# Kernel optimization log

Measured on AMD Instinct MI355X. Metric: run time of the kernel, lower is better.

Reference implementation:

```python
import jax, jax.numpy as jnp
import numpy as np

DX = 8e-6      # pixel pitch (m)
Z = 0.05       # propagation distance (m)
B, C, H, W = 8, 3, 1024, 1024


def setup_inputs() -> dict:
    key = jax.random.key(0)
    k1, k2 = jax.random.split(key)
    x_real = jax.random.normal(k1, (B, C, H, W), dtype=jnp.float32)
    x_imag = jax.random.normal(k2, (B, C, H, W), dtype=jnp.float32)
    wavelengths = jnp.asarray([450e-9, 532e-9, 632.8e-9], dtype=jnp.float32)
    return {"x_real": x_real, "x_imag": x_imag, "wavelengths": wavelengths}


def _transfer_function(wavelengths, h, w, dx, z):
    # Angular-spectrum transfer function per wavelength: [C, H, W] complex64
    fx = jnp.fft.fftfreq(w, d=dx).astype(jnp.float32)  # [W]
    fy = jnp.fft.fftfreq(h, d=dx).astype(jnp.float32)  # [H]
    f2 = fy[:, None] ** 2 + fx[None, :] ** 2           # [H, W]
    lam = wavelengths[:, None, None]                   # [C, 1, 1]
    arg = 1.0 - (lam ** 2) * f2[None]                  # [C, H, W]
    kz = (2.0 * jnp.pi / lam) * z * jnp.sqrt(jnp.maximum(arg, 0.0))
    Hc = jnp.exp(1j * kz.astype(jnp.complex64))
    # zero out evanescent components
    return jnp.where(arg > 0.0, Hc, jnp.zeros((), dtype=jnp.complex64))


def reference(x_real, x_imag, wavelengths):
    # Batched angular-spectrum propagation, one wavelength per channel.
    x = (x_real + 1j * x_imag).astype(jnp.complex64)   # [B, C, H, W]
    Hc = _transfer_function(wavelengths, H, W, DX, Z)  # [C, H, W]
    Xf = jnp.fft.fft2(x, axes=(-2, -1))
    out = jnp.fft.ifft2(Xf * Hc[None], axes=(-2, -1))  # [B, C, H, W] complex
    # return real/imag stacked so output is a float tensor: [2, B, C, H, W]
    return jnp.stack([out.real.astype(jnp.float32), out.imag.astype(jnp.float32)], axis=0)
```

## Files before the change

### kernel.cpp

```cpp
#include <hip/hip_runtime.h>
#include <math.h>


#define NIMG 24

__device__ __forceinline__ float2 cadd(float2 a, float2 b){ return make_float2(a.x+b.x, a.y+b.y); }
__device__ __forceinline__ float2 csub(float2 a, float2 b){ return make_float2(a.x-b.x, a.y-b.y); }
__device__ __forceinline__ float2 cmul(float2 a, float c, float s){ return make_float2(a.x*c - a.y*s, a.x*s + a.y*c); }

__device__ __forceinline__ int SW(int j) {
    int b = j << 3;
    return b ^ (((b >> 7) & 7) << 4);
}

__device__ __forceinline__ float2 computeH(float lam, int ky, int kx) {
    int iy = (ky < 512) ? ky : ky - 1024;
    int ix = (kx < 512) ? kx : kx - 1024;
    const double recip = 1.0 / (1024.0 * 8e-06);
    float fy = (float)((double)iy * recip);
    float fx = (float)((double)ix * recip);
    float f2  = __fadd_rn(__fmul_rn(fy, fy), __fmul_rn(fx, fx));
    float l2  = __fmul_rn(lam, lam);
    float arg = __fsub_rn(1.0f, __fmul_rn(l2, f2));
    float2 h = make_float2(0.0f, 0.0f);
    if (arg > 0.0f) {
        float t  = __fdiv_rn(6.28318530717958647692f, lam);
        t        = __fmul_rn(t, 0.05f);
        float kz = __fmul_rn(t, __fsqrt_rn(arg));
        double s, c;
        sincos((double)kz, &s, &c);
        const float sc = 9.5367431640625e-07f;
        h = make_float2((float)c * sc, (float)s * sc);
    }
    return h;
}

__global__ __launch_bounds__(256) void build_H_T(float2* __restrict__ Htab,
                                                 const float* __restrict__ wl) {
    int idx = blockIdx.x * 256 + threadIdx.x;
    int c   = idx >> 20;
    int rem = idx & 1048575;
    Htab[idx] = computeH(wl[c], rem & 1023, rem >> 10);
}

template<int SIGN>
__device__ __forceinline__ void dft4nt(float2& a0, float2& a1, float2& a2, float2& a3) {
    float2 t0 = cadd(a0, a2), t1 = csub(a0, a2);
    float2 t2 = cadd(a1, a3), t3 = csub(a1, a3);
    a0 = cadd(t0, t2);
    a2 = csub(t0, t2);
    a1 = make_float2(t1.x - SIGN * t3.y, t1.y + SIGN * t3.x);
    a3 = make_float2(t1.x + SIGN * t3.y, t1.y - SIGN * t3.x);
}
template<int SIGN>
__device__ __forceinline__ void dft4(float2& a0, float2& a1, float2& a2, float2& a3,
                                     float c1, float s1) {
    float c2 = c1*c1 - s1*s1, s2 = 2.f*c1*s1;
    float c3 = c2*c1 - s2*s1, s3 = s2*c1 + c2*s1;
    a1 = cmul(a1, c1, s1);
    a2 = cmul(a2, c2, s2);
    a3 = cmul(a3, c3, s3);
    dft4nt<SIGN>(a0, a1, a2, a3);
}

#define WSYNC() do { asm volatile("s_waitcnt lgkmcnt(0)" ::: "memory"); \
                     __builtin_amdgcn_wave_barrier(); } while (0)


__device__ __forceinline__ void ldsToRegs(char* cb, int l, float2 (&v)[4][4]) {
    const int swzE = (((l >> 4)    ) & 7) << 4;
    const int swzO = (((l >> 4) + 4) & 7) << 4;
    char* rbE = cb + ((8 * l) ^ swzE);
    char* rbO = cb + ((8 * l) ^ swzO);
    #pragma unroll
    for (int k = 0; k < 4; ++k) {
        #pragma unroll
        for (int r = 0; r < 4; ++r) {
            const int tt = k + 4 * r;
            v[k][r] = *(const float2*)(((tt & 1) ? rbO : rbE) + 512 * tt);
        }
    }
}
__device__ __forceinline__ void regsToLds(char* cb, int l, const float2 (&v)[4][4]) {
    const int swzE = (((l >> 4)    ) & 7) << 4;
    const int swzO = (((l >> 4) + 4) & 7) << 4;
    char* rbE = cb + ((8 * l) ^ swzE);
    char* rbO = cb + ((8 * l) ^ swzO);
    #pragma unroll
    for (int m = 0; m < 4; ++m) {
        #pragma unroll
        for (int q = 0; q < 4; ++q) {
            const int tt = m + 4 * q;
            *(float2*)(((tt & 1) ? rbO : rbE) + 512 * tt) = v[m][q];
        }
    }
}

template<int SIGN>
__device__ __forceinline__ void fftA(char* cb, int l, float2 (&v)[4][4]) {
    const float SPI8 = SIGN * 0.39269908169872415481f;
    #pragma unroll
    for (int k = 0; k < 4; ++k) dft4nt<SIGN>(v[k][0], v[k][1], v[k][2], v[k][3]);
    dft4nt<SIGN>(v[0][0], v[1][0], v[2][0], v[3][0]);
    #pragma unroll
    for (int q = 1; q < 4; ++q) {
        float s1, c1; __sincosf((float)q * SPI8, &s1, &c1);
        dft4<SIGN>(v[0][q], v[1][q], v[2][q], v[3][q], c1, s1);
    }
    char* wb = cb + 128 * l;
    const int L7 = l & 7;
    #pragma unroll
    for (int p = 0; p < 4; ++p) {
        *(float4*)(wb + 16 * ((2*p+0) ^ L7)) =
            make_float4(v[p][0].x, v[p][0].y, v[p][1].x, v[p][1].y);
        *(float4*)(wb + 16 * ((2*p+1) ^ L7)) =
            make_float4(v[p][2].x, v[p][2].y, v[p][3].x, v[p][3].y);
    }
}

template<int SIGN>
__device__ __forceinline__ void fftB(char* cb, int l) {
    const float SPI32  = SIGN * 0.09817477042468103870f;
    const float SPI128 = SIGN * 0.02454369260617025967f;
    const int swzE = (((l >> 4)    ) & 7) << 4;
    const int swzO = (((l >> 4) + 4) & 7) << 4;
    char* rbE = cb + ((8 * l) ^ swzE);
    char* rbO = cb + ((8 * l) ^ swzO);
    float2 v[4][4];
    #pragma unroll
    for (int k = 0; k < 4; ++k) {
        #pragma unroll
        for (int r = 0; r < 4; ++r) {
            const int tt = k + 4 * r;
            v[k][r] = *(const float2*)(((tt & 1) ? rbO : rbE) + 512 * tt);
        }
    }
    const int jm2 = l & 15;
    float s1, c1; __sincosf((float)jm2 * SPI32, &s1, &c1);
    #pragma unroll
    for (int k = 0; k < 4; ++k) dft4<SIGN>(v[k][0], v[k][1], v[k][2], v[k][3], c1, s1);
    const int lo8 = 8 * (l & 15);
    const int hi  = 2048 * (l >> 4);
    #pragma unroll
    for (int q = 0; q < 4; ++q) {
        float s1b, c1b; __sincosf((float)(jm2 + 16 * q) * SPI128, &s1b, &c1b);
        dft4<SIGN>(v[0][q], v[1][q], v[2][q], v[3][q], c1b, s1b);
        #pragma unroll
        for (int p = 0; p < 4; ++p) {
            const int K = ((q + 4 * p) & 7) << 4;
            *(float2*)(cb + (lo8 ^ K) + hi + 128 * q + 512 * p) = v[p][q];
        }
    }
}

template<int SIGN>
__device__ __forceinline__ void fftC(int l, float2 (&v)[4][4]) {
    const float SPI512 = SIGN * 0.00613592315154256492f;
    #pragma unroll
    for (int m = 0; m < 4; ++m) {
        float s1, c1; __sincosf((float)(l + 64 * m) * SPI512, &s1, &c1);
        dft4<SIGN>(v[m][0], v[m][1], v[m][2], v[m][3], c1, s1);
    }
}

__global__ __launch_bounds__(1024) void k1_rows_T16(const float* __restrict__ xr,
                                                    const float* __restrict__ xi,
                                                    float2* __restrict__ T) {
    extern __shared__ char lds[];
    const int t = threadIdx.x, w = t >> 6, l = t & 63;
    const int img = blockIdx.x >> 6;
    const int y0  = (blockIdx.x & 63) << 4;
    const long long ib = (long long)img << 20;
    char* cb = lds + 8192 * w;

    const float* rr = xr + ib + (long long)(y0 + w) * 1024;
    const float* ri = xi + ib + (long long)(y0 + w) * 1024;
    float2 v[4][4];
    #pragma unroll
    for (int k = 0; k < 4; ++k) {
        #pragma unroll
        for (int r = 0; r < 4; ++r) {
            const int p = l + 64 * (k + 4 * r);
            v[k][r] = make_float2(rr[p], ri[p]);
        }
    }
    fftA<-1>(cb, l, v); WSYNC();
    fftB<-1>(cb, l);    WSYNC();
    ldsToRegs(cb, l, v);
    fftC<-1>(l, v);
    __syncthreads();

    {
        const int w8 = w << 3;
        #pragma unroll
        for (int m = 0; m < 4; ++m) {
            #pragma unroll
            for (int q = 0; q < 4; ++q) {
                const int p  = l + 64 * (m + 4 * q);
                const int sx = (((p >> 1) & 7) << 4) | (((p >> 4) & 1) << 3);
                *(float2*)(lds + p * 128 + (w8 ^ sx)) = v[m][q];
            }
        }
    }
    __syncthreads();

    {
        const int j = l >> 3;
        const int xbase = (w << 3) + (l & 7);
        const bool sw = (w >> 1) & 1;
        #pragma unroll
        for (int i = 0; i < 8; ++i) {
            const int x   = xbase + (i << 7);
            const int s70 = ((x >> 1) & 7) << 4;
            float4 g = *(const float4*)(lds + x * 128 + ((16 * j) ^ s70));
            if (sw) g = make_float4(g.z, g.w, g.x, g.y);
            *(float4*)(T + ib + (long long)x * 1024 + y0 + 2 * j) = g;
        }
    }
}

__global__ __launch_bounds__(256, 4) void k2_cols_H(float2* __restrict__ T,
                                                    const float2* __restrict__ Htab,
                                                    const float* __restrict__ wl) {
    __shared__ float4 ldsb[2048];
    char* lds = (char*)ldsb;
    const int t = threadIdx.x, w = t >> 6, l = t & 63;
    const int img = blockIdx.x >> 8;
    const int x   = ((blockIdx.x & 255) << 2) + w;
    const int lamIdx = img % 3;
    char* cb = lds + 8192 * w;
    float2* col = T + ((long long)img << 20) + (long long)x * 1024;

    float2 v[4][4];
    #pragma unroll
    for (int k = 0; k < 4; ++k) {
        #pragma unroll
        for (int r = 0; r < 4; ++r)
            v[k][r] = col[l + 64 * (k + 4 * r)];
    }
    fftA<-1>(cb, l, v); WSYNC();
    fftB<-1>(cb, l);    WSYNC();

    float2 h[4][4];
    if (Htab) {
        const float2* hrow = Htab + ((long long)lamIdx << 20) + (long long)x * 1024;
        #pragma unroll
        for (int m = 0; m < 4; ++m) {
            #pragma unroll
            for (int q = 0; q < 4; ++q)
                h[m][q] = hrow[l + 64 * (m + 4 * q)];
        }
    } else {
        const float lam = wl[lamIdx];
        #pragma unroll
        for (int m = 0; m < 4; ++m) {
            #pragma unroll
            for (int q = 0; q < 4; ++q)
                h[m][q] = computeH(lam, l + 64 * (m + 4 * q), x);
        }
    }

    ldsToRegs(cb, l, v);
    fftC<-1>(l, v);

    #pragma unroll
    for (int m = 0; m < 4; ++m) {
        #pragma unroll
        for (int q = 0; q < 4; ++q) {
            float2 a = v[m][q], hh = h[m][q];
            v[m][q] = make_float2(a.x * hh.x - a.y * hh.y, a.x * hh.y + a.y * hh.x);
        }
    }
    WSYNC();

    fftA<1>(cb, l, v); WSYNC();
    fftB<1>(cb, l);    WSYNC();
    ldsToRegs(cb, l, v);
    fftC<1>(l, v);

    #pragma unroll
    for (int m = 0; m < 4; ++m) {
        #pragma unroll
        for (int q = 0; q < 4; ++q)
            col[l + 64 * (m + 4 * q)] = v[m][q];
    }
}

__global__ __launch_bounds__(1024) void k3_irows_T16(const float2* __restrict__ T,
                                                     float* __restrict__ outr,
                                                     float* __restrict__ outi) {
    extern __shared__ char lds[];
    const int t = threadIdx.x, w = t >> 6, l = t & 63;
    const int img = blockIdx.x >> 6;
    const int y0  = (blockIdx.x & 63) << 4;
    const long long ib = (long long)img << 20;

    {
        const float4* src = (const float4*)(T + ib + (long long)t * 1024 + y0);
        const int sx = SW(t);
        #pragma unroll
        for (int p = 0; p < 8; ++p) {
            float4 g = src[p];
            *(float2*)(lds + 8192 * (2 * p)     + sx) = make_float2(g.x, g.y);
            *(float2*)(lds + 8192 * (2 * p + 1) + sx) = make_float2(g.z, g.w);
        }
    }
    __syncthreads();

    char* cb = lds + 8192 * w;
    float2 v[4][4];
    ldsToRegs(cb, l, v);
    fftA<1>(cb, l, v); WSYNC();
    fftB<1>(cb, l);    WSYNC();
    ldsToRegs(cb, l, v);
    fftC<1>(l, v);

    float* pr = outr + ib + (long long)(y0 + w) * 1024;
    float* pi = outi + ib + (long long)(y0 + w) * 1024;
    #pragma unroll
    for (int m = 0; m < 4; ++m) {
        #pragma unroll
        for (int q = 0; q < 4; ++q) {
            const int p = l + 64 * (m + 4 * q);
            pr[p] = v[m][q].x;
            pi[p] = v[m][q].y;
        }
    }
}

extern "C" void kernel_launch(void* const* d_in, const int* in_sizes, int n_in,
                              void* d_out, int out_size, void* d_ws, size_t ws_size,
                              hipStream_t stream) {
    const float* xr = (const float*)d_in[0];
    const float* xi = (const float*)d_in[1];
    const float* wl = (const float*)d_in[2];
    float* out = (float*)d_out;

    const size_t planeElems = (size_t)NIMG * 1024 * 1024;
    float2* wsC = (float2*)d_ws;
    const size_t needC = planeElems * sizeof(float2);
    const size_t needH = (size_t)3 * 1024 * 1024 * sizeof(float2);
    float2* Htab = nullptr;
    if (ws_size >= needC + needH) {
        Htab = (float2*)((char*)d_ws + needC);
        build_H_T<<<12288, 256, 0, stream>>>(Htab, wl);
    }
    k1_rows_T16<<<NIMG * 64, 1024, 131072, stream>>>(xr, xi, wsC);
    k2_cols_H<<<NIMG * 256, 256, 0, stream>>>(wsC, Htab, wl);
    k3_irows_T16<<<NIMG * 64, 1024, 131072, stream>>>(wsC, out, out + planeElems);
}
```

Measured before the change: 304.2 us.

## Rotate 16-element row blocks in intermediate buffer to spread memory channels

The intermediate transposed buffer T now stores each 16-element block of a column at a position rotated by the column index, (b0 + x) & 63, instead of at y0. All three kernels are updated to match: the row-FFT writer, the column-FFT reader/writer via a CIDX mapping, and the inverse-row reader. The aim is to stop the strided transposed writes and reads from hitting the same memory channels or banks at the same time (partition camping). In exchange it adds index arithmetic, and the column kernel's loads become less regular, which could hurt coalescing within a wave.

Measured after the change: 350.2 us. 1.15x slower.

```diff
diff --git a/kernel.cpp b/kernel.cpp
--- a/kernel.cpp
+++ b/kernel.cpp
@@ -81,20 +81,6 @@
         }
     }
 }
-__device__ __forceinline__ void regsToLds(char* cb, int l, const float2 (&v)[4][4]) {
-    const int swzE = (((l >> 4)    ) & 7) << 4;
-    const int swzO = (((l >> 4) + 4) & 7) << 4;
-    char* rbE = cb + ((8 * l) ^ swzE);
-    char* rbO = cb + ((8 * l) ^ swzO);
-    #pragma unroll
-    for (int m = 0; m < 4; ++m) {
-        #pragma unroll
-        for (int q = 0; q < 4; ++q) {
-            const int tt = m + 4 * q;
-            *(float2*)(((tt & 1) ? rbO : rbE) + 512 * tt) = v[m][q];
-        }
-    }
-}
 
 template<int SIGN>
 __device__ __forceinline__ void fftA(char* cb, int l, float2 (&v)[4][4]) {
@@ -169,7 +155,8 @@
     extern __shared__ char lds[];
     const int t = threadIdx.x, w = t >> 6, l = t & 63;
     const int img = blockIdx.x >> 6;
-    const int y0  = (blockIdx.x & 63) << 4;
+    const int b0  = blockIdx.x & 63;
+    const int y0  = b0 << 4;
     const long long ib = (long long)img << 20;
     char* cb = lds + 8192 * w;
 
@@ -214,7 +201,8 @@
             const int s70 = ((x >> 1) & 7) << 4;
             float4 g = *(const float4*)(lds + x * 128 + ((16 * j) ^ s70));
             if (sw) g = make_float4(g.z, g.w, g.x, g.y);
-            *(float4*)(T + ib + (long long)x * 1024 + y0 + 2 * j) = g;
+            const int rb = (b0 + x) & 63;
+            *(float4*)(T + ib + (long long)x * 1024 + (rb << 4) + 2 * j) = g;
         }
     }
 }
@@ -231,12 +219,15 @@
     char* cb = lds + 8192 * w;
     float2* col = T + ((long long)img << 20) + (long long)x * 1024;
 
+    const int xl15 = l & 15, lhi = l >> 4;
+    #define CIDX(tt) (((((lhi) + 4 * (tt) + x) & 63) << 4) + xl15)
+
     float2 v[4][4];
     #pragma unroll
     for (int k = 0; k < 4; ++k) {
         #pragma unroll
         for (int r = 0; r < 4; ++r)
-            v[k][r] = col[l + 64 * (k + 4 * r)];
+            v[k][r] = col[CIDX(k + 4 * r)];
     }
     fftA<-1>(cb, l, v); WSYNC();
     fftB<-1>(cb, l);    WSYNC();
@@ -282,8 +273,9 @@
     for (int m = 0; m < 4; ++m) {
         #pragma unroll
         for (int q = 0; q < 4; ++q)
-            col[l + 64 * (m + 4 * q)] = v[m][q];
-    }
+            col[CIDX(m + 4 * q)] = v[m][q];
+    }
+    #undef CIDX
 }
 
 __global__ __launch_bounds__(1024) void k3_irows_T16(const float2* __restrict__ T,
@@ -292,11 +284,13 @@
     extern __shared__ char lds[];
     const int t = threadIdx.x, w = t >> 6, l = t & 63;
     const int img = blockIdx.x >> 6;
-    const int y0  = (blockIdx.x & 63) << 4;
+    const int b0  = blockIdx.x & 63;
+    const int y0  = b0 << 4;
     const long long ib = (long long)img << 20;
 
     {
-        const float4* src = (const float4*)(T + ib + (long long)t * 1024 + y0);
+        const int rb = (b0 + t) & 63;
+        const float4* src = (const float4*)(T + ib + (long long)t * 1024 + (rb << 4));
         const int sx = SW(t);
         #pragma unroll
         for (int p = 0; p < 8; ++p) {
```

## Use tiled 8-column panel layout between row and column FFT passes

Applied to the files above, without the earlier changes.

Row FFT kernel now uses 512-thread blocks of 8 rows and writes into a panel layout where each 8-column tile is stored contiguously, so the column kernel reads 8 adjacent columns per block with coalesced 64-byte segments instead of strided columns. The column kernel precomputes its stage twiddles once and reuses them across the forward and inverse FFTs, and fftA uses constant twiddles instead of sincos. When workspace allows, the column pass writes to a separate transposed buffer for the existing inverse-row kernel; otherwise it writes back in panel layout and a new panel-reading inverse-row kernel runs. This uses an extra full-size workspace buffer and changes occupancy and block shapes.

New measurement: 454.2 us. 49.3% more time.

```diff
diff --git a/kernel.cpp b/kernel.cpp
--- a/kernel.cpp
+++ b/kernel.cpp
@@ -10,6 +10,10 @@
 
 __device__ __forceinline__ int SW(int j) {
     int b = j << 3;
+    return b ^ (((b >> 7) & 7) << 4);
+}
+__device__ __forceinline__ int SW16(int a) {
+    int b = a << 4;
     return b ^ (((b >> 7) & 7) << 4);
 }
 
@@ -98,15 +102,15 @@
 
 template<int SIGN>
 __device__ __forceinline__ void fftA(char* cb, int l, float2 (&v)[4][4]) {
-    const float SPI8 = SIGN * 0.39269908169872415481f;
     #pragma unroll
     for (int k = 0; k < 4; ++k) dft4nt<SIGN>(v[k][0], v[k][1], v[k][2], v[k][3]);
     dft4nt<SIGN>(v[0][0], v[1][0], v[2][0], v[3][0]);
-    #pragma unroll
-    for (int q = 1; q < 4; ++q) {
-        float s1, c1; __sincosf((float)q * SPI8, &s1, &c1);
-        dft4<SIGN>(v[0][q], v[1][q], v[2][q], v[3][q], c1, s1);
-    }
+    dft4<SIGN>(v[0][1], v[1][1], v[2][1], v[3][1],
+               0.92387953251128674f, SIGN * 0.38268343236508978f);
+    dft4<SIGN>(v[0][2], v[1][2], v[2][2], v[3][2],
+               0.70710678118654752f, SIGN * 0.70710678118654752f);
+    dft4<SIGN>(v[0][3], v[1][3], v[2][3], v[3][3],
+               0.38268343236508978f, SIGN * 0.92387953251128674f);
     char* wb = cb + 128 * l;
     const int L7 = l & 7;
     #pragma unroll
@@ -154,6 +158,38 @@
 }
 
 template<int SIGN>
+__device__ __forceinline__ void fftB_tw(char* cb, int l, float cB, float sB,
+                                        const float (&cq)[4], const float (&sq)[4]) {
+    const int swzE = (((l >> 4)    ) & 7) << 4;
+    const int swzO = (((l >> 4) + 4) & 7) << 4;
+    char* rbE = cb + ((8 * l) ^ swzE);
+    char* rbO = cb + ((8 * l) ^ swzO);
+    float2 v[4][4];
+    #pragma unroll
+    for (int k = 0; k < 4; ++k) {
+        #pragma unroll
+        for (int r = 0; r < 4; ++r) {
+            const int tt = k + 4 * r;
+            v[k][r] = *(const float2*)(((tt & 1) ? rbO : rbE) + 512 * tt);
+        }
+    }
+    const float s1 = SIGN * sB;
+    #pragma unroll
+    for (int k = 0; k < 4; ++k) dft4<SIGN>(v[k][0], v[k][1], v[k][2], v[k][3], cB, s1);
+    const int lo8 = 8 * (l & 15);
+    const int hi  = 2048 * (l >> 4);
+    #pragma unroll
+    for (int q = 0; q < 4; ++q) {
+        dft4<SIGN>(v[0][q], v[1][q], v[2][q], v[3][q], cq[q], SIGN * sq[q]);
+        #pragma unroll
+        for (int p = 0; p < 4; ++p) {
+            const int K = ((q + 4 * p) & 7) << 4;
+            *(float2*)(cb + (lo8 ^ K) + hi + 128 * q + 512 * p) = v[p][q];
+        }
+    }
+}
+
+template<int SIGN>
 __device__ __forceinline__ void fftC(int l, float2 (&v)[4][4]) {
     const float SPI512 = SIGN * 0.00613592315154256492f;
     #pragma unroll
@@ -162,14 +198,22 @@
         dft4<SIGN>(v[m][0], v[m][1], v[m][2], v[m][3], c1, s1);
     }
 }
-
-__global__ __launch_bounds__(1024) void k1_rows_T16(const float* __restrict__ xr,
+template<int SIGN>
+__device__ __forceinline__ void fftC_tw(float2 (&v)[4][4],
+                                        const float (&cC)[4], const float (&sC)[4]) {
+    #pragma unroll
+    for (int m = 0; m < 4; ++m)
+        dft4<SIGN>(v[m][0], v[m][1], v[m][2], v[m][3], cC[m], SIGN * sC[m]);
+}
+
+__global__ __launch_bounds__(512, 4) void k1_rows_P(const float* __restrict__ xr,
                                                     const float* __restrict__ xi,
-                                                    float2* __restrict__ T) {
-    extern __shared__ char lds[];
+                                                    float2* __restrict__ P) {
+    __shared__ float4 ldsb[4096];
+    char* lds = (char*)ldsb;
     const int t = threadIdx.x, w = t >> 6, l = t & 63;
-    const int img = blockIdx.x >> 6;
-    const int y0  = (blockIdx.x & 63) << 4;
+    const int img = blockIdx.x >> 7;
+    const int y0  = (blockIdx.x & 127) << 3;
     const long long ib = (long long)img << 20;
     char* cb = lds + 8192 * w;
 
@@ -188,62 +232,59 @@
     fftB<-1>(cb, l);    WSYNC();
     ldsToRegs(cb, l, v);
     fftC<-1>(l, v);
+    WSYNC();
+    regsToLds(cb, l, v);
     __syncthreads();
 
     {
-        const int w8 = w << 3;
-        #pragma unroll
-        for (int m = 0; m < 4; ++m) {
-            #pragma unroll
-            for (int q = 0; q < 4; ++q) {
-                const int p  = l + 64 * (m + 4 * q);
-                const int sx = (((p >> 1) & 7) << 4) | (((p >> 4) & 1) << 3);
-                *(float2*)(lds + p * 128 + (w8 ^ sx)) = v[m][q];
-            }
-        }
-    }
-    __syncthreads();
-
-    {
-        const int j = l >> 3;
-        const int xbase = (w << 3) + (l & 7);
-        const bool sw = (w >> 1) & 1;
-        #pragma unroll
-        for (int i = 0; i < 8; ++i) {
-            const int x   = xbase + (i << 7);
-            const int s70 = ((x >> 1) & 7) << 4;
-            float4 g = *(const float4*)(lds + x * 128 + ((16 * j) ^ s70));
-            if (sw) g = make_float4(g.z, g.w, g.x, g.y);
-            *(float4*)(T + ib + (long long)x * 1024 + y0 + 2 * j) = g;
-        }
-    }
-}
-
-__global__ __launch_bounds__(256, 4) void k2_cols_H(float2* __restrict__ T,
+        const int xt = t >> 2, c2 = t & 3;
+        const int a  = xt * 4 + c2;
+        #pragma unroll
+        for (int k = 0; k < 8; ++k) {
+            float4 vv = *(const float4*)(lds + 8192 * k + SW16(a));
+            *(float4*)(P + ib + (long long)xt * 8192 + (y0 + k) * 8 + 2 * c2) = vv;
+        }
+    }
+}
+
+__global__ __launch_bounds__(512, 4) void k2_cols_P(float2* __restrict__ P,
+                                                    float2* __restrict__ Tout,
                                                     const float2* __restrict__ Htab,
                                                     const float* __restrict__ wl) {
-    __shared__ float4 ldsb[2048];
+    __shared__ float4 ldsb[4096];
     char* lds = (char*)ldsb;
     const int t = threadIdx.x, w = t >> 6, l = t & 63;
-    const int img = blockIdx.x >> 8;
-    const int x   = ((blockIdx.x & 255) << 2) + w;
+    const int img = blockIdx.x >> 7;
+    const int xt  = blockIdx.x & 127;
+    const int x   = (xt << 3) + w;
     const int lamIdx = img % 3;
     char* cb = lds + 8192 * w;
-    float2* col = T + ((long long)img << 20) + (long long)x * 1024;
+    const long long ib = (long long)img << 20;
+    float2* pcol = P + ib + (long long)xt * 8192 + w + 8 * l;
+
+    const int jm2 = l & 15;
+    float cB, sB; __sincosf((float)jm2 * 0.09817477042468103870f, &sB, &cB);
+    float cq[4], sq[4], cC[4], sC[4];
+    #pragma unroll
+    for (int q = 0; q < 4; ++q)
+        __sincosf((float)(jm2 + 16 * q) * 0.02454369260617025967f, &sq[q], &cq[q]);
+    #pragma unroll
+    for (int m = 0; m < 4; ++m)
+        __sincosf((float)(l + 64 * m) * 0.00613592315154256492f, &sC[m], &cC[m]);
 
     float2 v[4][4];
     #pragma unroll
     for (int k = 0; k < 4; ++k) {
         #pragma unroll
         for (int r = 0; r < 4; ++r)
-            v[k][r] = col[l + 64 * (k + 4 * r)];
-    }
-    fftA<-1>(cb, l, v); WSYNC();
-    fftB<-1>(cb, l);    WSYNC();
+            v[k][r] = pcol[512 * (k + 4 * r)];
+    }
+    fftA<-1>(cb, l, v);                WSYNC();
+    fftB_tw<-1>(cb, l, cB, sB, cq, sq); WSYNC();
 
     float2 h[4][4];
     if (Htab) {
-        const float2* hrow = Htab + ((long long)lamIdx << 20) + (long long)x * 1024;
+        const float2* hrow = Htab + ((long long)lamIdx << 20) + ((long long)x << 10);
         #pragma unroll
         for (int m = 0; m < 4; ++m) {
             #pragma unroll
@@ -261,7 +302,7 @@
     }
 
     ldsToRegs(cb, l, v);
-    fftC<-1>(l, v);
+    fftC_tw<-1>(v, cC, sC);
 
     #pragma unroll
     for (int m = 0; m < 4; ++m) {
@@ -273,16 +314,68 @@
     }
     WSYNC();
 
+    fftA<1>(cb, l, v);                 WSYNC();
+    fftB_tw<1>(cb, l, cB, sB, cq, sq); WSYNC();
+    ldsToRegs(cb, l, v);
+    fftC_tw<1>(v, cC, sC);
+
+    if (Tout) {
+        float2* tcol = Tout + ib + ((long long)x << 10);
+        #pragma unroll
+        for (int m = 0; m < 4; ++m) {
+            #pragma unroll
+            for (int q = 0; q < 4; ++q)
+                tcol[l + 64 * (m + 4 * q)] = v[m][q];
+        }
+    } else {
+        #pragma unroll
+        for (int m = 0; m < 4; ++m) {
+            #pragma unroll
+            for (int q = 0; q < 4; ++q)
+                pcol[512 * (m + 4 * q)] = v[m][q];
+        }
+    }
+}
+
+__global__ __launch_bounds__(512, 4) void k3_irows_P(const float2* __restrict__ P,
+                                                     float* __restrict__ outr,
+                                                     float* __restrict__ outi) {
+    __shared__ float4 ldsb[4096];
+    char* lds = (char*)ldsb;
+    const int t = threadIdx.x, w = t >> 6, l = t & 63;
+    const int img = blockIdx.x >> 7;
+    const int y0  = (blockIdx.x & 127) << 3;
+    const long long ib = (long long)img << 20;
+    char* cb = lds + 8192 * w;
+
+    {
+        const int xt = t >> 2, c2 = t & 3;
+        const int a  = xt * 4 + c2;
+        #pragma unroll
+        for (int k = 0; k < 8; ++k) {
+            float4 g = *(const float4*)(P + ib + (long long)xt * 8192 + (y0 + k) * 8 + 2 * c2);
+            *(float4*)(lds + 8192 * k + SW16(a)) = g;
+        }
+    }
+    __syncthreads();
+
+    float2 v[4][4];
+    ldsToRegs(cb, l, v);
     fftA<1>(cb, l, v); WSYNC();
     fftB<1>(cb, l);    WSYNC();
     ldsToRegs(cb, l, v);
     fftC<1>(l, v);
 
+    float* pr = outr + ib + (long long)(y0 + w) * 1024;
+    float* pi = outi + ib + (long long)(y0 + w) * 1024;
     #pragma unroll
     for (int m = 0; m < 4; ++m) {
         #pragma unroll
-        for (int q = 0; q < 4; ++q)
-            col[l + 64 * (m + 4 * q)] = v[m][q];
+        for (int q = 0; q < 4; ++q) {
+            const int p = l + 64 * (m + 4 * q);
+            pr[p] = v[m][q].x;
+            pi[p] = v[m][q].y;
+        }
     }
 }
 
@@ -296,7 +389,7 @@
     const long long ib = (long long)img << 20;
 
     {
-        const float4* src = (const float4*)(T + ib + (long long)t * 1024 + y0);
+        const float4* src = (const float4*)(T + ib + ((long long)t << 10) + y0);
         const int sx = SW(t);
         #pragma unroll
         for (int p = 0; p < 8; ++p) {
@@ -337,15 +430,28 @@
     float* out = (float*)d_out;
 
     const size_t planeElems = (size_t)NIMG * 1024 * 1024;
-    float2* wsC = (float2*)d_ws;
-    const size_t needC = planeElems * sizeof(float2);
+    const size_t needP = planeElems * sizeof(float2);
+    const size_t needT = needP;
     const size_t needH = (size_t)3 * 1024 * 1024 * sizeof(float2);
+
+    float2* P = (float2*)d_ws;
+    float2* T = nullptr;
     float2* Htab = nullptr;
-    if (ws_size >= needC + needH) {
-        Htab = (float2*)((char*)d_ws + needC);
+
+    if (ws_size >= needP + needT + needH) {
+        T    = (float2*)((char*)d_ws + needP);
+        Htab = (float2*)((char*)d_ws + needP + needT);
         build_H_T<<<12288, 256, 0, stream>>>(Htab, wl);
-    }
-    k1_rows_T16<<<NIMG * 64, 1024, 131072, stream>>>(xr, xi, wsC);
-    k2_cols_H<<<NIMG * 256, 256, 0, stream>>>(wsC, Htab, wl);
-    k3_irows_T16<<<NIMG * 64, 1024, 131072, stream>>>(wsC, out, out + planeElems);
-}
+    } else if (ws_size >= needP + needH) {
+        Htab = (float2*)((char*)d_ws + needP);
+        build_H_T<<<12288, 256, 0, stream>>>(Htab, wl);
+    }
+
+    k1_rows_P<<<NIMG * 128, 512, 0, stream>>>(xr, xi, P);
+    k2_cols_P<<<NIMG * 128, 512, 0, stream>>>(P, T, Htab, wl);
+    if (T) {
+        k3_irows_T16<<<NIMG * 64, 1024, 131072, stream>>>(T, out, out + planeElems);
+    } else {
+        k3_irows_P<<<NIMG * 128, 512, 0, stream>>>(P, out, out + planeElems);
+    }
+}
```
